# Kernel optimization log

Measured on AMD Instinct MI355X. Metric: run time of the kernel, lower is better.

Reference implementation:

```python
import jax, jax.numpy as jnp
import numpy as np

DIM = 1024
N_HEADS = 16
HEAD_DIM = DIM // N_HEADS
EPS = 1e-05
ROPE_BASE = 1000000.0


def apply_rope(x, base=ROPE_BASE):
    # x: [b, seq, heads, head_dim]
    b, seq, n_heads, dim = x.shape
    half = dim // 2
    i = jnp.arange(half)
    theta = 1.0 / base ** (2 * i / dim)
    pos = jnp.arange(seq)
    angles = pos[:, None] * theta[None, :]            # [seq, half]
    cos = jnp.cos(angles)[None, :, None, :]           # [1, seq, 1, half]
    sin = jnp.sin(angles)[None, :, None, :]
    x1, x2 = jnp.split(x, 2, axis=-1)
    return jnp.concatenate([x1 * cos - x2 * sin, x1 * sin + x2 * cos], axis=-1)


def setup_inputs() -> dict:
    key = jax.random.key(0)
    ks = jax.random.split(key, 6)
    b, seq = 2, 2048
    scale = 1.0 / np.sqrt(DIM)
    x = jax.random.normal(ks[0], (b, seq, DIM), dtype=jnp.float32)
    w_norm = jnp.ones((DIM,), dtype=jnp.float32)
    Wq = jax.random.normal(ks[1], (DIM, DIM), dtype=jnp.float32) * scale
    Wk = jax.random.normal(ks[2], (DIM, DIM), dtype=jnp.float32) * scale
    Wv = jax.random.normal(ks[3], (DIM, DIM), dtype=jnp.float32) * scale
    Wo = jax.random.normal(ks[4], (DIM, DIM), dtype=jnp.float32) * scale
    return {"x": x, "w_norm": w_norm, "Wq": Wq, "Wk": Wk, "Wv": Wv, "Wo": Wo}


def reference(x, w_norm, Wq, Wk, Wv, Wo):
    b, seq, d = x.shape
    # RMSNorm
    rms = jnp.sqrt(jnp.mean(x * x, axis=-1, keepdims=True) + EPS)
    x_norm = x / rms * w_norm
    # QKV projections (Dense without bias: y = x @ W)
    q = (x_norm @ Wq).reshape(b, seq, N_HEADS, HEAD_DIM)
    k = (x_norm @ Wk).reshape(b, seq, N_HEADS, HEAD_DIM)
    v = (x_norm @ Wv).reshape(b, seq, N_HEADS, HEAD_DIM)
    q = apply_rope(q)
    k = apply_rope(k)
    # Causal attention with full [b,h,t,s] scores (faithful to source)
    scores = jnp.einsum('bthd,bshd->bhts', q, k) / jnp.sqrt(jnp.float32(HEAD_DIM))
    causal = jnp.triu(jnp.full((seq, seq), -jnp.inf, dtype=scores.dtype), k=1)
    scores = scores + causal[None, None, :, :]
    attn = jax.nn.softmax(scores, axis=-1)
    out = jnp.einsum('bhts,bshd->bthd', attn, v).reshape(b, seq, d)
    return out @ Wo
```

## Files before the change

### kernel.cpp

```cpp
#include <hip/hip_runtime.h>

#define DIM 1024
#define SEQ 2048
#define BATCH 2
#define NHEADS 16
#define HD 64
#define ROWS (BATCH * SEQ)

typedef __bf16 bf16x8 __attribute__((ext_vector_type(8)));
typedef __bf16 bf16x4 __attribute__((ext_vector_type(4)));
typedef float f32x4 __attribute__((ext_vector_type(4)));
typedef float f32x16 __attribute__((ext_vector_type(16)));
typedef unsigned u32x4 __attribute__((ext_vector_type(4)));

__device__ __forceinline__ f32x4 f4zero() {
    f32x4 z = {0.f, 0.f, 0.f, 0.f};
    return z;
}

__device__ __forceinline__ unsigned cvtpk(float lo, float hi) {
    unsigned r;
    asm("v_cvt_pk_bf16_f32 %0, %1, %2" : "=v"(r) : "v"(lo), "v"(hi));
    return r;
}

__device__ __forceinline__ void pl32swap(unsigned& a, unsigned& b) {
    asm volatile("v_permlane32_swap_b32 %0, %1" : "+v"(a), "+v"(b));
}

__device__ __forceinline__ float fexp2(float x) {
    float r;
    asm("v_exp_f32 %0, %1" : "=v"(r) : "v"(x));
    return r;
}

#define GLOAD_LDS16(g, l)                                                                  \
    __builtin_amdgcn_global_load_lds((const __attribute__((address_space(1))) void*)(g),   \
                                     (__attribute__((address_space(3))) void*)(l), 16, 0, 0)

__global__ __launch_bounds__(256) void rmsnorm_bf16(const float* __restrict__ x,
                                                    const float* __restrict__ w,
                                                    __bf16* __restrict__ xn) {
    int row = blockIdx.x;
    int t = threadIdx.x;
    float4 v = ((const float4*)(x + (size_t)row * DIM))[t];
    float ss = v.x * v.x + v.y * v.y + v.z * v.z + v.w * v.w;
#pragma unroll
    for (int off = 1; off < 64; off <<= 1) ss += __shfl_xor(ss, off);
    __shared__ float red[4];
    if ((t & 63) == 0) red[t >> 6] = ss;
    __syncthreads();
    ss = red[0] + red[1] + red[2] + red[3];
    float scale = rsqrtf(ss * (1.0f / DIM) + 1e-5f);
    float4 wv = ((const float4*)w)[t];
    bf16x4 o;
    o[0] = (__bf16)(v.x * scale * wv.x);
    o[1] = (__bf16)(v.y * scale * wv.y);
    o[2] = (__bf16)(v.z * scale * wv.z);
    o[3] = (__bf16)(v.w * scale * wv.w);
    *(bf16x4*)(xn + (size_t)row * DIM + t * 4) = o;
}

__global__ __launch_bounds__(256) void wcvt_kernel(const float* __restrict__ Wq,
                                                   const float* __restrict__ Wk,
                                                   const float* __restrict__ Wv,
                                                   const float* __restrict__ Wo,
                                                   __bf16* tq, __bf16* tk, __bf16* tv, __bf16* to_) {
    int z = blockIdx.z;
    const float* W = z == 0 ? Wq : z == 1 ? Wk : z == 2 ? Wv : Wo;
    __bf16* T = z == 0 ? tq : z == 1 ? tk : z == 2 ? tv : to_;
    __shared__ float tile[32][33];
    int n0 = blockIdx.x * 32, k0 = blockIdx.y * 32;
    int tx = threadIdx.x & 31, ty = threadIdx.x >> 5;
#pragma unroll
    for (int j = 0; j < 32; j += 8) tile[ty + j][tx] = W[(size_t)(k0 + ty + j) * DIM + n0 + tx];
    __syncthreads();
#pragma unroll
    for (int j = 0; j < 32; j += 8)
        T[(size_t)(n0 + ty + j) * DIM + k0 + tx] = (__bf16)tile[tx][ty + j];
}

__global__ __launch_bounds__(256) void rope_table_kernel(float* __restrict__ cosT,
                                                         float* __restrict__ sinT) {
    int idx = blockIdx.x * 256 + threadIdx.x;
    int s = idx >> 5, i = idx & 31;
    float e = (2.0f * (float)i) / 64.0f;
    float theta = 1.0f / powf(1000000.0f, e);
    float ang = (float)s * theta;
    cosT[idx] = cosf(ang);
    sinT[idx] = sinf(ang);
}

__device__ __forceinline__ void gemm_core(const __bf16* __restrict__ A,
                                          const __bf16* __restrict__ Bt,
                                          int K, __bf16* As, __bf16* Bs,
                                          f32x4 (&acc)[4][4], int row0, int col0) {
    int tid = threadIdx.x;
    int w = tid >> 6, l = tid & 63, l15 = l & 15, g = l >> 4;
    int wr = (w >> 1) << 6, wc = (w & 1) << 6;

    int sr0 = tid >> 2;
    int sr1 = 64 + (tid >> 2);
    int lc0 = (((tid & 3) ^ ((tid >> 3) & 3)) << 3);
    const __bf16* gA0 = A + (size_t)(row0 + sr0) * K + lc0;
    const __bf16* gA1 = A + (size_t)(row0 + sr1) * K + lc0;
    const __bf16* gB0 = Bt + (size_t)(col0 + sr0) * K + lc0;
    const __bf16* gB1 = Bt + (size_t)(col0 + sr1) * K + lc0;
    __bf16* lA0 = As + w * 512;
    __bf16* lA1 = As + 2048 + w * 512;
    __bf16* lB0 = Bs + w * 512;
    __bf16* lB1 = Bs + 2048 + w * 512;

    int rca = ((g ^ ((l15 >> 1) & 3)) << 3);

#pragma unroll
    for (int i = 0; i < 4; ++i)
#pragma unroll
        for (int j = 0; j < 4; ++j) acc[i][j] = f4zero();

    for (int k0 = 0; k0 < K; k0 += 32) {
        __syncthreads();
        GLOAD_LDS16(gA0 + k0, lA0);
        GLOAD_LDS16(gA1 + k0, lA1);
        GLOAD_LDS16(gB0 + k0, lB0);
        GLOAD_LDS16(gB1 + k0, lB1);
        __syncthreads();

        bf16x8 af[4], bfr[4];
#pragma unroll
        for (int i = 0; i < 4; ++i) af[i] = *(const bf16x8*)&As[(wr + i * 16 + l15) * 32 + rca];
#pragma unroll
        for (int j = 0; j < 4; ++j) bfr[j] = *(const bf16x8*)&Bs[(wc + j * 16 + l15) * 32 + rca];
        __builtin_amdgcn_s_setprio(1);
#pragma unroll
        for (int i = 0; i < 4; ++i)
#pragma unroll
            for (int j = 0; j < 4; ++j)
                acc[i][j] = __builtin_amdgcn_mfma_f32_16x16x32_bf16(af[i], bfr[j], acc[i][j], 0, 0, 0);
        __builtin_amdgcn_s_setprio(0);
    }
}

__global__ __launch_bounds__(256) void gemm_qkv_kernel(const __bf16* __restrict__ xn,
                                                       const __bf16* __restrict__ wq,
                                                       const __bf16* __restrict__ wk,
                                                       const __bf16* __restrict__ wv,
                                                       __bf16* __restrict__ qf,
                                                       __bf16* __restrict__ kf,
                                                       __bf16* __restrict__ vf,
                                                       const float* __restrict__ cosT,
                                                       const float* __restrict__ sinT) {
    __shared__ __bf16 smem[9216];
    __bf16* As = smem;
    __bf16* Bs = smem + 4096;
    int bid = blockIdx.x;
    int tid = threadIdx.x;
    int w = tid >> 6, l = tid & 63, l15 = l & 15, gq = l >> 4;
    int l31 = l & 31, hi = l >> 5;
    int wr = (w >> 1) << 6, wc = (w & 1) << 6;
    __bf16* Ls = smem + w * 2304;
    f32x4 acc[4][4];

    if (bid < 512) {
        int z = bid >> 8, t = bid & 255;
        int col0 = (t & 7) << 7, row0 = (t >> 3) << 7;
        gemm_core(xn, z ? wk : wq, DIM, As, Bs, acc, row0, col0);
        __syncthreads();
        __bf16* F = z ? kf : qf;
        int colbase = col0 + wc;
        int hh = colbase >> 6;
        int row0w = row0 + wr;
        int bb = row0w >> 11;
        int bh = bb * 16 + hh;
        int tbase = (row0w & (SEQ - 1)) >> 5;
#pragma unroll
        for (int p = 0; p < 2; ++p) {
#pragma unroll
            for (int i = 0; i < 4; ++i) {
#pragma unroll
                for (int r = 0; r < 4; ++r) {
                    int row64 = i * 16 + gq * 4 + r;
                    int s = (row0w + row64) & (SEQ - 1);
#pragma unroll
                    for (int jj = 0; jj < 2; ++jj) {
                        float c = cosT[s * 32 + jj * 16 + l15];
                        float sn = sinT[s * 32 + jj * 16 + l15];
                        float val;
                        if (p == 0)
                            val = acc[i][jj][r] * c - acc[i][jj + 2][r] * sn;
                        else
                            val = acc[i][jj][r] * sn + acc[i][jj + 2][r] * c;
                        Ls[row64 * 36 + jj * 16 + l15] = (__bf16)val;
                    }
                }
            }
#pragma unroll
            for (int si = 0; si < 2; ++si) {
#pragma unroll
                for (int gg = 0; gg < 2; ++gg) {
                    int g = 2 * p + gg;
                    bf16x8 v = *(const bf16x8*)&Ls[(si * 32 + l31) * 36 + gg * 16 + hi * 8];
                    size_t dst = (((size_t)(bh * 64 + tbase + si) * 4 + g) * 64 + l) * 8;
                    *(bf16x8*)&F[dst] = v;
                }
            }
        }
    } else {
        int t = bid - 512;
        int b = t >> 7, r7 = t & 127;
        int row0 = (r7 >> 4) << 7;
        int col0 = (r7 & 15) << 7;
        gemm_core(wv, xn + (size_t)b * SEQ * DIM, DIM, As, Bs, acc, row0, col0);
        __syncthreads();
        int hh = (row0 + wr) >> 6;
        int bh = b * 16 + hh;
#pragma unroll
        for (int p = 0; p < 2; ++p) {
#pragma unroll
            for (int i = 0; i < 4; ++i) {
#pragma unroll
                for (int r = 0; r < 4; ++r) {
                    int row64 = i * 16 + gq * 4 + r;
#pragma unroll
                    for (int jj = 0; jj < 2; ++jj)
                        Ls[row64 * 36 + jj * 16 + l15] = (__bf16)acc[i][2 * p + jj][r];
                }
            }
            int t32 = ((col0 + wc) >> 5) + p;
#pragma unroll
            for (int half = 0; half < 2; ++half) {
#pragma unroll
                for (int kk = 0; kk < 2; ++kk) {
                    bf16x8 v = *(const bf16x8*)&Ls[(half * 32 + l31) * 36 + kk * 16 + hi * 8];
                    size_t dst = ((((size_t)(bh * 64 + t32) * 2 + half) * 2 + kk) * 64 + l) * 8;
                    *(bf16x8*)&vf[dst] = v;
                }
            }
        }
    }
}

__global__ __launch_bounds__(256) void gemm_out_kernel(const __bf16* __restrict__ ctx,
                                                       const __bf16* __restrict__ wo,
                                                       float* __restrict__ out) {
    __shared__ __bf16 As[128 * 32];
    __shared__ __bf16 Bs[128 * 32];
    int row0 = (int)blockIdx.y << 7, col0 = (int)blockIdx.x << 7;
    f32x4 acc[4][4];
    gemm_core(ctx, wo, DIM, As, Bs, acc, row0, col0);
    int tid = threadIdx.x;
    int w = tid >> 6, l = tid & 63, l15 = l & 15, g = l >> 4;
    int wr = (w >> 1) << 6, wc = (w & 1) << 6;
#pragma unroll
    for (int i = 0; i < 4; ++i)
#pragma unroll
        for (int j = 0; j < 4; ++j)
#pragma unroll
            for (int r = 0; r < 4; ++r) {
                int row = row0 + wr + i * 16 + g * 4 + r;
                int col = col0 + wc + j * 16 + l15;
                out[(size_t)row * DIM + col] = acc[i][j][r];
            }
}

__global__ __launch_bounds__(256, 3) void attn_mfma_kernel(const __bf16* __restrict__ qf,
                                                           const __bf16* __restrict__ kf,
                                                           const __bf16* __restrict__ vf,
                                                           __bf16* __restrict__ part_O,
                                                           float* __restrict__ part_ml) {
    int bh = blockIdx.x;
    int tid = threadIdx.x, wvx = tid >> 6, l = tid & 63;
    int wslot = (int)blockIdx.y * 4 + wvx;
    int slot = 95 - wslot;
    int qp, ci;
    if (slot < 32) {
        qp = slot;
        ci = 0;
    } else {
        int t = slot - 32;
        qp = 32 + (t >> 1);
        ci = t & 1;
    }
    int rem = qp - (ci << 5);
    int ntiles = rem < 32 ? rem + 1 : 32;
    int dtile = rem < 32 ? rem : -1;
    int t0 = ci << 5;

    int l31 = l & 31, hi = l >> 5;
    int qrow = qp * 32 + l31;

    bf16x8 qfr[4];
    {
        const __bf16* qp_ = qf + ((size_t)bh * 64 + qp) * 2048 + (size_t)l * 8;
        const float c2 = 0.125f * 1.44269504f;
#pragma unroll
        for (int g = 0; g < 4; ++g) {
            bf16x8 tq = *(const bf16x8*)(qp_ + g * 512);
#pragma unroll
            for (int e = 0; e < 8; ++e) qfr[g][e] = (__bf16)((float)tq[e] * c2);
        }
    }

    const __bf16* kfp = kf + ((size_t)bh * 64 + t0) * 2048 + (size_t)l * 8;
    const __bf16* vfp = vf + ((size_t)bh * 64 + t0) * 2048 + (size_t)l * 8;

    f32x16 oA, oB;
#pragma unroll
    for (int r = 0; r < 16; ++r) {
        oA[r] = 0.f;
        oB[r] = 0.f;
    }
    float m_run = -1e30f, l_run = 0.f;

    bf16x8 ka[4], kb[4];
#pragma unroll
    for (int g = 0; g < 4; ++g) ka[g] = *(const bf16x8*)(kfp + g * 512);

    auto tile_body = [&](bf16x8 (&kcur)[4], bf16x8 (&knxt)[4], int st) {
        if (st + 1 < ntiles) {
            const __bf16* kn = kfp + (size_t)(st + 1) * 2048;
#pragma unroll
            for (int g = 0; g < 4; ++g) knxt[g] = *(const bf16x8*)(kn + g * 512);
        }
        const __bf16* vp = vfp + (size_t)st * 2048;
        bf16x8 v00 = *(const bf16x8*)(vp);
        bf16x8 v01 = *(const bf16x8*)(vp + 512);
        bf16x8 v10 = *(const bf16x8*)(vp + 1024);
        bf16x8 v11 = *(const bf16x8*)(vp + 1536);

        f32x16 sa;
#pragma unroll
        for (int r = 0; r < 16; ++r) sa[r] = 0.f;
        __builtin_amdgcn_s_setprio(1);
#pragma unroll
        for (int g = 0; g < 4; ++g)
            sa = __builtin_amdgcn_mfma_f32_32x32x16_bf16(kcur[g], qfr[g], sa, 0, 0, 0);
        __builtin_amdgcn_s_setprio(0);

        if (st == dtile) {
            int s0 = (t0 + st) << 5;
#pragma unroll
            for (int r = 0; r < 16; ++r) {
                int kg = s0 + (r & 3) + 8 * (r >> 2) + 4 * hi;
                if (kg > qrow) sa[r] = -1e30f;
            }
        }

        float mx[8];
#pragma unroll
        for (int r = 0; r < 8; ++r) mx[r] = fmaxf(sa[r], sa[r + 8]);
#pragma unroll
        for (int r = 0; r < 4; ++r) mx[r] = fmaxf(mx[r], mx[r + 4]);
        float lmax = fmaxf(fmaxf(mx[0], mx[1]), fmaxf(mx[2], mx[3]));
        if (!__all(lmax <= m_run + 10.0f)) {
            float omax = fmaxf(lmax, __shfl_xor(lmax, 32));
            float m_new = fmaxf(m_run, omax);
            float alpha = fexp2(m_run - m_new);
            l_run *= alpha;
#pragma unroll
            for (int r = 0; r < 16; ++r) {
                oA[r] *= alpha;
                oB[r] *= alpha;
            }
            m_run = m_new;
        }
#pragma unroll
        for (int r = 0; r < 16; ++r) sa[r] = fexp2(sa[r] - m_run);
        float s8[8];
#pragma unroll
        for (int r = 0; r < 8; ++r) s8[r] = sa[r] + sa[r + 8];
#pragma unroll
        for (int r = 0; r < 4; ++r) s8[r] += s8[r + 4];
        float ls = (s8[0] + s8[1]) + (s8[2] + s8[3]);
        l_run += ls + __shfl_xor(ls, 32);

        unsigned a0 = cvtpk(sa[0], sa[1]), b0 = cvtpk(sa[4], sa[5]);
        pl32swap(a0, b0);
        unsigned c0 = cvtpk(sa[2], sa[3]), d0 = cvtpk(sa[6], sa[7]);
        pl32swap(c0, d0);
        u32x4 t4a = {a0, c0, b0, d0};
        bf16x8 pa0 = __builtin_bit_cast(bf16x8, t4a);
        unsigned a1 = cvtpk(sa[8], sa[9]), b1 = cvtpk(sa[12], sa[13]);
        pl32swap(a1, b1);
        unsigned c1 = cvtpk(sa[10], sa[11]), d1 = cvtpk(sa[14], sa[15]);
        pl32swap(c1, d1);
        u32x4 t4b = {a1, c1, b1, d1};
        bf16x8 pa1 = __builtin_bit_cast(bf16x8, t4b);

        __builtin_amdgcn_s_setprio(1);
        oA = __builtin_amdgcn_mfma_f32_32x32x16_bf16(v00, pa0, oA, 0, 0, 0);
        oA = __builtin_amdgcn_mfma_f32_32x32x16_bf16(v01, pa1, oA, 0, 0, 0);
        oB = __builtin_amdgcn_mfma_f32_32x32x16_bf16(v10, pa0, oB, 0, 0, 0);
        oB = __builtin_amdgcn_mfma_f32_32x32x16_bf16(v11, pa1, oB, 0, 0, 0);
        __builtin_amdgcn_s_setprio(0);
    };

    int st = 0;
    while (st < ntiles) {
        tile_body(ka, kb, st);
        ++st;
        if (st >= ntiles) break;
        tile_body(kb, ka, st);
        ++st;
    }

    int gslot = bh * 96 + slot;
    __bf16* po = part_O + (size_t)gslot * 2048 + l31 * 64;
#pragma unroll
    for (int rr = 0; rr < 16; rr += 4) {
        int d0 = 8 * (rr >> 2) + 4 * hi;
        uint2 pA = {cvtpk(oA[rr], oA[rr + 1]), cvtpk(oA[rr + 2], oA[rr + 3])};
        uint2 pB = {cvtpk(oB[rr], oB[rr + 1]), cvtpk(oB[rr + 2], oB[rr + 3])};
        *(uint2*)&po[d0] = pA;
        *(uint2*)&po[32 + d0] = pB;
    }
    if (hi == 0) {
        part_ml[(size_t)gslot * 64 + l31] = m_run;
        part_ml[(size_t)gslot * 64 + 32 + l31] = l_run;
    }
}

__global__ __launch_bounds__(128) void attn_combine_kernel(const __bf16* __restrict__ part_O,
                                                           const float* __restrict__ part_ml,
                                                           __bf16* __restrict__ ctx) {
    int bh = blockIdx.x, qp = blockIdx.y;
    int b = bh >> 4, h = bh & 15;
    int nch = 1 + (qp >> 5);
    int base = qp < 32 ? qp : 32 + 2 * (qp - 32);
    size_t so = (size_t)bh * 96 + base;
    int t = threadIdx.x;
    int row = t >> 2, dseg = (t & 3) << 4;

    float mv0 = part_ml[so * 64 + row];
    float mv1 = -1e30f;
    if (nch > 1) mv1 = part_ml[(so + 1) * 64 + row];
    float mmax = fmaxf(mv0, mv1);

    float acc[16];
#pragma unroll
    for (int e = 0; e < 16; ++e) acc[e] = 0.f;
    float lsum = 0.f;

#pragma unroll 2
    for (int i = 0; i < 2; ++i) {
        if (i >= nch) break;
        float mi = i == 0 ? mv0 : mv1;
        float wsc = fexp2(mi - mmax);
        lsum += wsc * part_ml[(so + i) * 64 + 32 + row];
        const __bf16* po = part_O + (so + i) * 2048 + row * 64 + dseg;
        bf16x8 a = *(const bf16x8*)po;
        bf16x8 b2 = *(const bf16x8*)(po + 8);
#pragma unroll
        for (int e = 0; e < 8; ++e) {
            acc[e] += wsc * (float)a[e];
            acc[8 + e] += wsc * (float)b2[e];
        }
    }

    float inv = 1.0f / lsum;
    bf16x8 oa, ob;
#pragma unroll
    for (int e = 0; e < 8; ++e) {
        oa[e] = (__bf16)(acc[e] * inv);
        ob[e] = (__bf16)(acc[8 + e] * inv);
    }
    size_t off = ((size_t)(b * SEQ) + qp * 32 + row) * DIM + h * HD + dseg;
    *(bf16x8*)&ctx[off] = oa;
    *(bf16x8*)&ctx[off + 8] = ob;
}

extern "C" void kernel_launch(void* const* d_in, const int* in_sizes, int n_in,
                              void* d_out, int out_size, void* d_ws, size_t ws_size,
                              hipStream_t stream) {
    const float* x = (const float*)d_in[0];
    const float* w_norm = (const float*)d_in[1];
    const float* Wq = (const float*)d_in[2];
    const float* Wk = (const float*)d_in[3];
    const float* Wv = (const float*)d_in[4];
    const float* Wo = (const float*)d_in[5];
    float* out = (float*)d_out;
    char* w8 = (char*)d_ws;

    const size_t MB = 1ull << 20;
    __bf16* xn = (__bf16*)(w8);
    __bf16* wtq = (__bf16*)(w8 + 8 * MB);
    __bf16* wtk = (__bf16*)(w8 + 10 * MB);
    __bf16* wtv = (__bf16*)(w8 + 12 * MB);
    __bf16* part_O = (__bf16*)(w8);
    float* part_ml = (float*)(w8 + 12 * MB);
    __bf16* wto = (__bf16*)(w8 + 14 * MB);
    __bf16* qf = (__bf16*)(w8 + 16 * MB);
    __bf16* kf = (__bf16*)(w8 + 24 * MB);
    __bf16* vf = (__bf16*)(w8 + 32 * MB);
    __bf16* ctx = (__bf16*)(w8 + 40 * MB);
    float* cosT = (float*)(w8 + 48 * MB);
    float* sinT = cosT + SEQ * 32;

    wcvt_kernel<<<dim3(32, 32, 4), 256, 0, stream>>>(Wq, Wk, Wv, Wo, wtq, wtk, wtv, wto);
    rmsnorm_bf16<<<ROWS, 256, 0, stream>>>(x, w_norm, xn);
    rope_table_kernel<<<(SEQ * 32) / 256, 256, 0, stream>>>(cosT, sinT);

    gemm_qkv_kernel<<<768, 256, 0, stream>>>(xn, wtq, wtk, wtv, qf, kf, vf, cosT, sinT);

    attn_mfma_kernel<<<dim3(BATCH * NHEADS, 24), 256, 0, stream>>>(qf, kf, vf, part_O, part_ml);
    attn_combine_kernel<<<dim3(BATCH * NHEADS, SEQ / 32), 128, 0, stream>>>(part_O, part_ml, ctx);

    gemm_out_kernel<<<dim3(DIM / 128, ROWS / 128), 256, 0, stream>>>(ctx, wto, out);
}
```

Before: 139.0 us.

## Double GEMM K-tile to 64 with XOR swizzle, block remap, nontemporal stores

The shared GEMM core now stages a 64-wide K slice per iteration with an 8-way XOR-swizzled LDS layout. This halves the number of barrier pairs and runs two MFMA sub-steps per load. The QKV and output GEMM block indices are permuted so that consecutive blocks spread across XCD-like groups, and epilogue stores become nontemporal. The cost is a larger LDS footprint, which may reduce occupancy, and a risk that nontemporal stores hurt the later kernels that read q/k/v.

```diff
diff --git a/kernel.cpp b/kernel.cpp
--- a/kernel.cpp
+++ b/kernel.cpp
@@ -91,53 +91,54 @@
     sinT[idx] = sinf(ang);
 }
 
-__device__ __forceinline__ void gemm_core(const __bf16* __restrict__ A,
-                                          const __bf16* __restrict__ Bt,
-                                          int K, __bf16* As, __bf16* Bs,
-                                          f32x4 (&acc)[4][4], int row0, int col0) {
+__device__ __forceinline__ void gemm_core64(const __bf16* __restrict__ A,
+                                            const __bf16* __restrict__ Bt,
+                                            int K, __bf16* As, __bf16* Bs,
+                                            f32x4 (&acc)[4][4], int row0, int col0) {
     int tid = threadIdx.x;
     int w = tid >> 6, l = tid & 63, l15 = l & 15, g = l >> 4;
     int wr = (w >> 1) << 6, wc = (w & 1) << 6;
 
-    int sr0 = tid >> 2;
-    int sr1 = 64 + (tid >> 2);
-    int lc0 = (((tid & 3) ^ ((tid >> 3) & 3)) << 3);
-    const __bf16* gA0 = A + (size_t)(row0 + sr0) * K + lc0;
-    const __bf16* gA1 = A + (size_t)(row0 + sr1) * K + lc0;
-    const __bf16* gB0 = Bt + (size_t)(col0 + sr0) * K + lc0;
-    const __bf16* gB1 = Bt + (size_t)(col0 + sr1) * K + lc0;
-    __bf16* lA0 = As + w * 512;
-    __bf16* lA1 = As + 2048 + w * 512;
-    __bf16* lB0 = Bs + w * 512;
-    __bf16* lB1 = Bs + 2048 + w * 512;
-
-    int rca = ((g ^ ((l15 >> 1) & 3)) << 3);
+    int srow = tid >> 3;
+    int schunk = ((tid & 7) ^ (srow & 7)) << 3;
+    const __bf16* gA = A + (size_t)(row0 + srow) * K + schunk;
+    const __bf16* gB = Bt + (size_t)(col0 + srow) * K + schunk;
+    __bf16* lA = As + w * 512;
+    __bf16* lB = Bs + w * 512;
 
 #pragma unroll
     for (int i = 0; i < 4; ++i)
 #pragma unroll
         for (int j = 0; j < 4; ++j) acc[i][j] = f4zero();
 
-    for (int k0 = 0; k0 < K; k0 += 32) {
+    int xr = (l15 & 7);
+    for (int k0 = 0; k0 < K; k0 += 64) {
         __syncthreads();
-        GLOAD_LDS16(gA0 + k0, lA0);
-        GLOAD_LDS16(gA1 + k0, lA1);
-        GLOAD_LDS16(gB0 + k0, lB0);
-        GLOAD_LDS16(gB1 + k0, lB1);
+#pragma unroll
+        for (int c = 0; c < 4; ++c) {
+            GLOAD_LDS16(gA + (size_t)(c * 32) * K + k0, lA + c * 2048);
+            GLOAD_LDS16(gB + (size_t)(c * 32) * K + k0, lB + c * 2048);
+        }
         __syncthreads();
-
-        bf16x8 af[4], bfr[4];
-#pragma unroll
-        for (int i = 0; i < 4; ++i) af[i] = *(const bf16x8*)&As[(wr + i * 16 + l15) * 32 + rca];
-#pragma unroll
-        for (int j = 0; j < 4; ++j) bfr[j] = *(const bf16x8*)&Bs[(wc + j * 16 + l15) * 32 + rca];
-        __builtin_amdgcn_s_setprio(1);
-#pragma unroll
-        for (int i = 0; i < 4; ++i)
+#pragma unroll
+        for (int kk = 0; kk < 2; ++kk) {
+            int q8 = kk * 4 + g;
+            int rc = (q8 ^ xr) << 3;
+            bf16x8 af[4], bfr[4];
+#pragma unroll
+            for (int i = 0; i < 4; ++i)
+                af[i] = *(const bf16x8*)&As[(wr + i * 16 + l15) * 64 + rc];
 #pragma unroll
             for (int j = 0; j < 4; ++j)
-                acc[i][j] = __builtin_amdgcn_mfma_f32_16x16x32_bf16(af[i], bfr[j], acc[i][j], 0, 0, 0);
-        __builtin_amdgcn_s_setprio(0);
+                bfr[j] = *(const bf16x8*)&Bs[(wc + j * 16 + l15) * 64 + rc];
+            __builtin_amdgcn_s_setprio(1);
+#pragma unroll
+            for (int i = 0; i < 4; ++i)
+#pragma unroll
+                for (int j = 0; j < 4; ++j)
+                    acc[i][j] = __builtin_amdgcn_mfma_f32_16x16x32_bf16(af[i], bfr[j], acc[i][j], 0, 0, 0);
+            __builtin_amdgcn_s_setprio(0);
+        }
     }
 }
 
@@ -150,10 +151,11 @@
                                                        __bf16* __restrict__ vf,
                                                        const float* __restrict__ cosT,
                                                        const float* __restrict__ sinT) {
-    __shared__ __bf16 smem[9216];
+    __shared__ __bf16 smem[16384];
     __bf16* As = smem;
-    __bf16* Bs = smem + 4096;
-    int bid = blockIdx.x;
+    __bf16* Bs = smem + 8192;
+    int bid0 = blockIdx.x;
+    int bid = ((bid0 & 7) * 96) + (bid0 >> 3);
     int tid = threadIdx.x;
     int w = tid >> 6, l = tid & 63, l15 = l & 15, gq = l >> 4;
     int l31 = l & 31, hi = l >> 5;
@@ -164,7 +166,7 @@
     if (bid < 512) {
         int z = bid >> 8, t = bid & 255;
         int col0 = (t & 7) << 7, row0 = (t >> 3) << 7;
-        gemm_core(xn, z ? wk : wq, DIM, As, Bs, acc, row0, col0);
+        gemm_core64(xn, z ? wk : wq, DIM, As, Bs, acc, row0, col0);
         __syncthreads();
         __bf16* F = z ? kf : qf;
         int colbase = col0 + wc;
@@ -201,7 +203,7 @@
                     int g = 2 * p + gg;
                     bf16x8 v = *(const bf16x8*)&Ls[(si * 32 + l31) * 36 + gg * 16 + hi * 8];
                     size_t dst = (((size_t)(bh * 64 + tbase + si) * 4 + g) * 64 + l) * 8;
-                    *(bf16x8*)&F[dst] = v;
+                    __builtin_nontemporal_store(v, (bf16x8*)&F[dst]);
                 }
             }
         }
@@ -210,7 +212,7 @@
         int b = t >> 7, r7 = t & 127;
         int row0 = (r7 >> 4) << 7;
         int col0 = (r7 & 15) << 7;
-        gemm_core(wv, xn + (size_t)b * SEQ * DIM, DIM, As, Bs, acc, row0, col0);
+        gemm_core64(wv, xn + (size_t)b * SEQ * DIM, DIM, As, Bs, acc, row0, col0);
         __syncthreads();
         int hh = (row0 + wr) >> 6;
         int bh = b * 16 + hh;
@@ -233,7 +235,7 @@
                 for (int kk = 0; kk < 2; ++kk) {
                     bf16x8 v = *(const bf16x8*)&Ls[(half * 32 + l31) * 36 + kk * 16 + hi * 8];
                     size_t dst = ((((size_t)(bh * 64 + t32) * 2 + half) * 2 + kk) * 64 + l) * 8;
-                    *(bf16x8*)&vf[dst] = v;
+                    __builtin_nontemporal_store(v, (bf16x8*)&vf[dst]);
                 }
             }
         }
@@ -243,11 +245,13 @@
 __global__ __launch_bounds__(256) void gemm_out_kernel(const __bf16* __restrict__ ctx,
                                                        const __bf16* __restrict__ wo,
                                                        float* __restrict__ out) {
-    __shared__ __bf16 As[128 * 32];
-    __shared__ __bf16 Bs[128 * 32];
-    int row0 = (int)blockIdx.y << 7, col0 = (int)blockIdx.x << 7;
+    __shared__ __bf16 As[8192];
+    __shared__ __bf16 Bs[8192];
+    int b0 = blockIdx.x;
+    int t = ((b0 & 7) * 32) + (b0 >> 3);
+    int row0 = (t >> 3) << 7, col0 = (t & 7) << 7;
     f32x4 acc[4][4];
-    gemm_core(ctx, wo, DIM, As, Bs, acc, row0, col0);
+    gemm_core64(ctx, wo, DIM, As, Bs, acc, row0, col0);
     int tid = threadIdx.x;
     int w = tid >> 6, l = tid & 63, l15 = l & 15, g = l >> 4;
     int wr = (w >> 1) << 6, wc = (w & 1) << 6;
@@ -259,7 +263,7 @@
             for (int r = 0; r < 4; ++r) {
                 int row = row0 + wr + i * 16 + g * 4 + r;
                 int col = col0 + wc + j * 16 + l15;
-                out[(size_t)row * DIM + col] = acc[i][j][r];
+                __builtin_nontemporal_store(acc[i][j][r], &out[(size_t)row * DIM + col]);
             }
 }
 
@@ -505,5 +509,5 @@
     attn_mfma_kernel<<<dim3(BATCH * NHEADS, 24), 256, 0, stream>>>(qf, kf, vf, part_O, part_ml);
     attn_combine_kernel<<<dim3(BATCH * NHEADS, SEQ / 32), 128, 0, stream>>>(part_O, part_ml, ctx);
 
-    gemm_out_kernel<<<dim3(DIM / 128, ROWS / 128), 256, 0, stream>>>(ctx, wto, out);
-}
+    gemm_out_kernel<<<256, 256, 0, stream>>>(ctx, wto, out);
+}
```

After: 134.3 us. -3.4%, faster.
